# Kernel tuning notes

Hardware: AMD Instinct MI355X
Metric: run time of the kernel (lower is better)

## Reference

```python
import jax, jax.numpy as jnp
import numpy as np

N_NODES = 50000
N_EDGES = 600000
D = 128
THETA = (0.5, -1.0, 0.5)  # len(theta) must be 3 to match learnable_diag[3, in_feats]


def setup_inputs() -> dict:
    key = jax.random.key(0)
    k1, k2, k3, k4, k5 = jax.random.split(key, 5)
    feat = jax.random.normal(k1, (N_NODES, D), dtype=jnp.float32)
    edge_index = jax.random.randint(k2, (2, N_EDGES), 0, N_NODES)  # [src; dst]
    # learnable_diag = torch.rand(3, in_feats)
    diag = jax.random.uniform(k3, (3, D), dtype=jnp.float32)
    # nn.Linear(out_feats, out_feats) with xavier_uniform weight, zero bias
    limit = float(np.sqrt(6.0 / (D + D)))
    W = jax.random.uniform(k4, (D, D), dtype=jnp.float32, minval=-limit, maxval=limit)
    b = jnp.zeros((D,), dtype=jnp.float32)
    return {"feat": feat, "edge_index": edge_index, "diag": diag, "W": W, "b": b}


def reference(feat, edge_index, diag, W, b):
    src, dst = edge_index[0], edge_index[1]
    n = feat.shape[0]
    # in_degrees: count of incoming edges per node
    deg = jax.ops.segment_sum(jnp.ones_like(dst, dtype=feat.dtype), dst, num_segments=n)
    d_invsqrt = jnp.clip(deg, 1.0, None) ** -0.5  # [N]
    d_invsqrt = d_invsqrt[:, None]  # [N,1]

    h = (THETA[0] * feat) * diag[0]
    h = h @ W.T + b  # nn.Linear

    for k in range(1, len(THETA)):
        # unnLaplacian: feat - (A @ (feat * Dinv)) * Dinv * diag[k]
        msg = feat * d_invsqrt  # [N,D]
        agg = jax.ops.segment_sum(msg[src], dst, num_segments=n)  # SpMM: copy_u + sum
        feat = feat - agg * d_invsqrt * diag[k]
        h = h + THETA[k] * feat
    return h
```

## Files before the change

### kernel.cpp

```cpp
#include <hip/hip_runtime.h>

#define NN 50000
#define NE 600000
#define D  128
#define NBLK 196

typedef __attribute__((ext_vector_type(8))) short bf16x8;
typedef __attribute__((ext_vector_type(4))) float floatx4;

__device__ __forceinline__ unsigned short bf16_rne(float f) {
    union { float f; unsigned u; } v; v.f = f;
    unsigned r = v.u + 0x7FFFu + ((v.u >> 16) & 1u);
    return (unsigned short)(r >> 16);
}
__device__ __forceinline__ unsigned pack2(float a, float b) {
    return (unsigned)bf16_rne(a) | ((unsigned)bf16_rne(b) << 16);
}

__global__ __launch_bounds__(256) void hist_kernel(const int* __restrict__ dst,
                                                   int* __restrict__ deg_i) {
    int e = blockIdx.x * 256 + threadIdx.x;
    if (e < NE) atomicAdd(&deg_i[dst[e]], 1);
}

__global__ __launch_bounds__(256) void scan1_kernel(const int* __restrict__ deg_i,
                                                    int* __restrict__ row_ptr,
                                                    int* __restrict__ partials,
                                                    float* __restrict__ dinvf,
                                                    float* __restrict__ rdegf) {
    __shared__ int sh[256];
    int i = blockIdx.x * 256 + threadIdx.x;
    int dg = (i < NN) ? deg_i[i] : 0;
    if (i < NN) {
        float d = (float)dg;
        float dc = d > 1.0f ? d : 1.0f;
        dinvf[i] = rsqrtf(dc);
        rdegf[i] = sqrtf(dc);
    }
    sh[threadIdx.x] = dg;
    __syncthreads();
    #pragma unroll
    for (int off = 1; off < 256; off <<= 1) {
        int t = (threadIdx.x >= off) ? sh[threadIdx.x - off] : 0;
        __syncthreads();
        sh[threadIdx.x] += t;
        __syncthreads();
    }
    if (i < NN) row_ptr[i + 1] = sh[threadIdx.x];
    if (threadIdx.x == 255) partials[blockIdx.x] = sh[255];
}

__global__ __launch_bounds__(256) void scan2_kernel(int* __restrict__ partials) {
    __shared__ int sh[256];
    sh[threadIdx.x] = (threadIdx.x < NBLK) ? partials[threadIdx.x] : 0;
    __syncthreads();
    #pragma unroll
    for (int off = 1; off < 256; off <<= 1) {
        int t = (threadIdx.x >= off) ? sh[threadIdx.x - off] : 0;
        __syncthreads();
        sh[threadIdx.x] += t;
        __syncthreads();
    }
    if (threadIdx.x < NBLK) partials[threadIdx.x] = sh[threadIdx.x];
}

__global__ __launch_bounds__(256) void scan3_kernel(int* __restrict__ row_ptr,
                                                    const int* __restrict__ partials,
                                                    int* __restrict__ fillc) {
    int i = blockIdx.x * 256 + threadIdx.x;
    if (i < NN) {
        int add = (blockIdx.x > 0) ? partials[blockIdx.x - 1] : 0;
        row_ptr[i + 1] += add;
        fillc[i] = 0;
    }
    if (i == 0) row_ptr[0] = 0;
}

__global__ __launch_bounds__(256) void fill_kernel(const int* __restrict__ src,
                                                   const int* __restrict__ dst,
                                                   const int* __restrict__ row_ptr,
                                                   int* __restrict__ fillc,
                                                   int* __restrict__ csr) {
    int e = blockIdx.x * 256 + threadIdx.x;
    if (e < NE) {
        int t = dst[e];
        int pos = row_ptr[t] + atomicAdd(&fillc[t], 1);
        csr[pos] = src[e];
    }
}

__global__ __launch_bounds__(256) void wprep_kernel(const float* __restrict__ W,
                                                    const float* __restrict__ diag,
                                                    unsigned short* __restrict__ Wb) {
    int idx = blockIdx.x * 256 + threadIdx.x;
    int j = idx & 127;
    Wb[idx] = bf16_rne(0.5f * diag[j] * W[idx]);
}

__global__ __launch_bounds__(256) void gemm_mfma_kernel(const float* __restrict__ feat,
                                                        const unsigned short* __restrict__ Wb,
                                                        const float* __restrict__ b,
                                                        const float* __restrict__ dinvf,
                                                        unsigned short* __restrict__ featb_s,
                                                        float* __restrict__ out) {
    const int wv   = threadIdx.x >> 6;
    const int lane = threadIdx.x & 63;
    const int r16  = lane & 15;
    const int quad = lane >> 4;
    const int m0   = blockIdx.x * 64 + wv * 16;

    const int mrow = m0 + r16;
    const int mc   = (mrow < NN) ? mrow : (NN - 1);
    const float* arow = feat + (size_t)mc * D + quad * 8;
    const float di = dinvf[mc];

    bf16x8 afrag[4];
    #pragma unroll
    for (int kc = 0; kc < 4; ++kc) {
        const float4 f0 = *(const float4*)(arow + kc * 32);
        const float4 f1 = *(const float4*)(arow + kc * 32 + 4);
        bf16x8 a;
        a[0] = (short)bf16_rne(f0.x); a[1] = (short)bf16_rne(f0.y);
        a[2] = (short)bf16_rne(f0.z); a[3] = (short)bf16_rne(f0.w);
        a[4] = (short)bf16_rne(f1.x); a[5] = (short)bf16_rne(f1.y);
        a[6] = (short)bf16_rne(f1.z); a[7] = (short)bf16_rne(f1.w);
        afrag[kc] = a;
        if (mrow < NN) {
            uint4 st;
            st.x = pack2(f0.x * di, f0.y * di);
            st.y = pack2(f0.z * di, f0.w * di);
            st.z = pack2(f1.x * di, f1.y * di);
            st.w = pack2(f1.z * di, f1.w * di);
            *(uint4*)(featb_s + (size_t)mc * D + quad * 8 + kc * 32) = st;
        }
    }

    floatx4 acc[8];
    #pragma unroll
    for (int nt = 0; nt < 8; ++nt) acc[nt] = (floatx4)(0.0f);

    #pragma unroll
    for (int nt = 0; nt < 8; ++nt) {
        const unsigned short* brow = Wb + (size_t)(nt * 16 + r16) * D + quad * 8;
        #pragma unroll
        for (int kc = 0; kc < 4; ++kc) {
            const bf16x8 bfrag = *(const bf16x8*)(brow + kc * 32);
            acc[nt] = __builtin_amdgcn_mfma_f32_16x16x32_bf16(afrag[kc], bfrag, acc[nt], 0, 0, 0);
        }
    }

    #pragma unroll
    for (int nt = 0; nt < 8; ++nt) {
        const int d = nt * 16 + r16;
        const float bd = b[d];
        #pragma unroll
        for (int r = 0; r < 4; ++r) {
            const int i = m0 + quad * 4 + r;
            if (i < NN) out[(size_t)i * D + d] = acc[nt][r] + bd;
        }
    }
}

__device__ __forceinline__ float2 gather_acc(const unsigned short* __restrict__ rows,
                                             const int* __restrict__ csr,
                                             int e0, int e1, int lane) {
    float2 acc = make_float2(0.0f, 0.0f);
    for (int bse = e0; bse < e1; bse += 64) {
        int idx = bse + lane;
        int s = (idx < e1) ? csr[idx] : NN;
        int cnt8 = (min(64, e1 - bse) + 7) & ~7;
        for (int k = 0; k < cnt8; k += 8) {
            #pragma unroll
            for (int u = 0; u < 8; ++u) {
                int ss = __shfl(s, k + u);
                unsigned pv = *(const unsigned*)(rows + (size_t)ss * D + 2 * lane);
                acc.x += __uint_as_float(pv << 16);
                acc.y += __uint_as_float(pv & 0xFFFF0000u);
            }
        }
    }
    return acc;
}

__global__ __launch_bounds__(256) void gather1_kernel(const unsigned short* __restrict__ featb_s,
                                                      const int* __restrict__ csr,
                                                      const int* __restrict__ row_ptr,
                                                      const float* __restrict__ dinvf,
                                                      const float* __restrict__ diag,
                                                      const float* __restrict__ feat0,
                                                      unsigned int* __restrict__ feat1s) {
    const int node = blockIdx.x * 4 + (threadIdx.x >> 6);
    const int lane = threadIdx.x & 63;
    float2 acc = gather_acc(featb_s, csr, row_ptr[node], row_ptr[node + 1], lane);

    const size_t o2 = (size_t)node * (D / 2) + lane;
    const float di = dinvf[node];
    const float2 bs = *(const float2*)&feat0[2 * o2];
    const float2 dg = *(const float2*)&diag[D + 2 * lane];
    float rx = bs.x - acc.x * di * dg.x;
    float ry = bs.y - acc.y * di * dg.y;
    feat1s[o2] = pack2(rx * di, ry * di);
}

__global__ __launch_bounds__(256) void gather2_kernel(const unsigned short* __restrict__ feat1s,
                                                      const int* __restrict__ csr,
                                                      const int* __restrict__ row_ptr,
                                                      const float* __restrict__ dinvf,
                                                      const float* __restrict__ rdegf,
                                                      const float* __restrict__ diag,
                                                      float* __restrict__ outp) {
    const int node = blockIdx.x * 4 + (threadIdx.x >> 6);
    const int lane = threadIdx.x & 63;
    float2 acc = gather_acc(feat1s, csr, row_ptr[node], row_ptr[node + 1], lane);

    const size_t o2 = (size_t)node * (D / 2) + lane;
    const float di = dinvf[node];
    const float rd = rdegf[node];
    const unsigned bp = ((const unsigned*)feat1s)[o2];
    const float2 dg = *(const float2*)&diag[2 * D + 2 * lane];
    float bx = __uint_as_float(bp << 16) * rd;
    float by = __uint_as_float(bp & 0xFFFF0000u) * rd;
    float2 cur = *(const float2*)&outp[2 * o2];
    cur.x -= 0.5f * (bx + acc.x * di * dg.x);
    cur.y -= 0.5f * (by + acc.y * di * dg.y);
    *(float2*)&outp[2 * o2] = cur;
}

extern "C" void kernel_launch(void* const* d_in, const int* in_sizes, int n_in,
                              void* d_out, int out_size, void* d_ws, size_t ws_size,
                              hipStream_t stream) {
    const float* feat = (const float*)d_in[0];
    const int*   eidx = (const int*)d_in[1];
    const float* diag = (const float*)d_in[2];
    const float* W    = (const float*)d_in[3];
    const float* b    = (const float*)d_in[4];
    float* out = (float*)d_out;

    const int* src = eidx;
    const int* dst = eidx + NE;

    unsigned short* featb_s = (unsigned short*)d_ws;
    unsigned short* feat1s  = featb_s + (size_t)(NN + 1) * D;
    int*   csr      = (int*)(feat1s + (size_t)(NN + 1) * D);
    float* dinvf    = (float*)(csr + NE);
    float* rdegf    = dinvf + NN;
    int*   deg_i    = (int*)(rdegf + NN);
    int*   row_ptr  = deg_i + NN;
    int*   fillc    = row_ptr + NN + 2;
    int*   partials = fillc + NN;
    unsigned short* Wb = (unsigned short*)(partials + 256);

    hipMemsetAsync(deg_i, 0, (size_t)NN * sizeof(int), stream);
    hipMemsetAsync(featb_s + (size_t)NN * D, 0, D * sizeof(unsigned short), stream);
    hipMemsetAsync(feat1s  + (size_t)NN * D, 0, D * sizeof(unsigned short), stream);

    hist_kernel<<<(NE + 255) / 256, 256, 0, stream>>>(dst, deg_i);
    scan1_kernel<<<NBLK, 256, 0, stream>>>(deg_i, row_ptr, partials, dinvf, rdegf);
    scan2_kernel<<<1, 256, 0, stream>>>(partials);
    scan3_kernel<<<NBLK, 256, 0, stream>>>(row_ptr, partials, fillc);
    fill_kernel<<<(NE + 255) / 256, 256, 0, stream>>>(src, dst, row_ptr, fillc, csr);

    wprep_kernel<<<64, 256, 0, stream>>>(W, diag, Wb);

    gemm_mfma_kernel<<<(NN + 63) / 64, 256, 0, stream>>>(feat, Wb, b, dinvf, featb_s, out);

    gather1_kernel<<<NN / 4, 256, 0, stream>>>(featb_s, csr, row_ptr, dinvf, diag,
                                               feat, (unsigned int*)feat1s);
    gather2_kernel<<<NN / 4, 256, 0, stream>>>(feat1s, csr, row_ptr, dinvf, rdegf, diag, out);
}
```

Baseline: 235.3 us.

## Fuse memsets and scans into fewer kernels and split gathers by feature half

Replaces the three memsets and the weight-prep kernel with one prep kernel. It also merges the three-pass scan into a single-pass decoupled look-back scan that uses per-block descriptors. The two gather kernels now launch twice as many blocks: each wave handles half of the feature dimension, and its two 32-lane halves walk alternate edges before combining with a cross-lane shuffle. This cuts launch overhead and raises memory-level parallelism in the gathers, at the cost of reading the CSR twice and relying on inter-block spin-waiting in the scan.

```diff
diff --git a/kernel.cpp b/kernel.cpp
--- a/kernel.cpp
+++ b/kernel.cpp
@@ -17,19 +17,40 @@
     return (unsigned)bf16_rne(a) | ((unsigned)bf16_rne(b) << 16);
 }
 
+__global__ __launch_bounds__(256) void prep_kernel(const float* __restrict__ W,
+                                                   const float* __restrict__ diag,
+                                                   unsigned short* __restrict__ Wb,
+                                                   int* __restrict__ deg_i,
+                                                   int* __restrict__ fillc,
+                                                   unsigned long long* __restrict__ desc,
+                                                   unsigned int* __restrict__ zrow0,
+                                                   unsigned int* __restrict__ zrow1) {
+    int g = blockIdx.x * 256 + threadIdx.x;
+    if (g < NN) { deg_i[g] = 0; fillc[g] = 0; }
+    if (g < 16384) {
+        int j = g & 127;
+        Wb[g] = bf16_rne(0.5f * diag[j] * W[g]);
+    }
+    if (g < 256) desc[g] = 0ULL;
+    if (g < 64) { zrow0[g] = 0u; zrow1[g] = 0u; }
+}
+
 __global__ __launch_bounds__(256) void hist_kernel(const int* __restrict__ dst,
                                                    int* __restrict__ deg_i) {
     int e = blockIdx.x * 256 + threadIdx.x;
     if (e < NE) atomicAdd(&deg_i[dst[e]], 1);
 }
 
-__global__ __launch_bounds__(256) void scan1_kernel(const int* __restrict__ deg_i,
-                                                    int* __restrict__ row_ptr,
-                                                    int* __restrict__ partials,
-                                                    float* __restrict__ dinvf,
-                                                    float* __restrict__ rdegf) {
+__global__ __launch_bounds__(256) void scan_kernel(const int* __restrict__ deg_i,
+                                                   int* __restrict__ row_ptr,
+                                                   unsigned long long* __restrict__ desc,
+                                                   float* __restrict__ dinvf,
+                                                   float* __restrict__ rdegf) {
     __shared__ int sh[256];
-    int i = blockIdx.x * 256 + threadIdx.x;
+    __shared__ int exc_sh;
+    const int b = blockIdx.x;
+    const int t = threadIdx.x;
+    const int i = b * 256 + t;
     int dg = (i < NN) ? deg_i[i] : 0;
     if (i < NN) {
         float d = (float)dg;
@@ -37,42 +58,41 @@
         dinvf[i] = rsqrtf(dc);
         rdegf[i] = sqrtf(dc);
     }
-    sh[threadIdx.x] = dg;
+    sh[t] = dg;
     __syncthreads();
     #pragma unroll
     for (int off = 1; off < 256; off <<= 1) {
-        int t = (threadIdx.x >= off) ? sh[threadIdx.x - off] : 0;
+        int v = (t >= off) ? sh[t - off] : 0;
         __syncthreads();
-        sh[threadIdx.x] += t;
+        sh[t] += v;
         __syncthreads();
     }
-    if (i < NN) row_ptr[i + 1] = sh[threadIdx.x];
-    if (threadIdx.x == 255) partials[blockIdx.x] = sh[255];
-}
-
-__global__ __launch_bounds__(256) void scan2_kernel(int* __restrict__ partials) {
-    __shared__ int sh[256];
-    sh[threadIdx.x] = (threadIdx.x < NBLK) ? partials[threadIdx.x] : 0;
+    if (t == 0) {
+        const int agg = sh[255];
+        if (b == 0) {
+            exc_sh = 0;
+            atomicExch(&desc[0], (2ULL << 32) | (unsigned)agg);
+        } else {
+            atomicExch(&desc[b], (1ULL << 32) | (unsigned)agg);
+            long long running = 0;
+            int p = b - 1;
+            for (;;) {
+                unsigned long long v;
+                do {
+                    v = atomicAdd(&desc[p], 0ULL);
+                    if ((v >> 32) == 0) __builtin_amdgcn_s_sleep(1);
+                } while ((v >> 32) == 0);
+                running += (long long)(unsigned)v;
+                if ((v >> 32) == 2ULL) break;
+                --p;
+            }
+            exc_sh = (int)running;
+            atomicExch(&desc[b], (2ULL << 32) | (unsigned)(running + agg));
+        }
+    }
     __syncthreads();
-    #pragma unroll
-    for (int off = 1; off < 256; off <<= 1) {
-        int t = (threadIdx.x >= off) ? sh[threadIdx.x - off] : 0;
-        __syncthreads();
-        sh[threadIdx.x] += t;
-        __syncthreads();
-    }
-    if (threadIdx.x < NBLK) partials[threadIdx.x] = sh[threadIdx.x];
-}
-
-__global__ __launch_bounds__(256) void scan3_kernel(int* __restrict__ row_ptr,
-                                                    const int* __restrict__ partials,
-                                                    int* __restrict__ fillc) {
-    int i = blockIdx.x * 256 + threadIdx.x;
-    if (i < NN) {
-        int add = (blockIdx.x > 0) ? partials[blockIdx.x - 1] : 0;
-        row_ptr[i + 1] += add;
-        fillc[i] = 0;
-    }
+    const int exc = exc_sh;
+    if (i < NN) row_ptr[i + 1] = sh[t] + exc;
     if (i == 0) row_ptr[0] = 0;
 }
 
@@ -87,14 +107,6 @@
         int pos = row_ptr[t] + atomicAdd(&fillc[t], 1);
         csr[pos] = src[e];
     }
-}
-
-__global__ __launch_bounds__(256) void wprep_kernel(const float* __restrict__ W,
-                                                    const float* __restrict__ diag,
-                                                    unsigned short* __restrict__ Wb) {
-    int idx = blockIdx.x * 256 + threadIdx.x;
-    int j = idx & 127;
-    Wb[idx] = bf16_rne(0.5f * diag[j] * W[idx]);
 }
 
 __global__ __launch_bounds__(256) void gemm_mfma_kernel(const float* __restrict__ feat,
@@ -161,9 +173,11 @@
     }
 }
 
-__device__ __forceinline__ float2 gather_acc(const unsigned short* __restrict__ rows,
-                                             const int* __restrict__ csr,
-                                             int e0, int e1, int lane) {
+__device__ __forceinline__ float2 gather_half(const unsigned short* __restrict__ rows,
+                                              const int* __restrict__ csr,
+                                              int e0, int e1, int lane, int half) {
+    const unsigned short* rbase = rows + half * 64 + 2 * (lane & 31);
+    const int sub = lane >> 5;
     float2 acc = make_float2(0.0f, 0.0f);
     for (int bse = e0; bse < e1; bse += 64) {
         int idx = bse + lane;
@@ -171,14 +185,16 @@
         int cnt8 = (min(64, e1 - bse) + 7) & ~7;
         for (int k = 0; k < cnt8; k += 8) {
             #pragma unroll
-            for (int u = 0; u < 8; ++u) {
-                int ss = __shfl(s, k + u);
-                unsigned pv = *(const unsigned*)(rows + (size_t)ss * D + 2 * lane);
+            for (int u = 0; u < 8; u += 2) {
+                int ss = __shfl(s, k + u + sub);
+                unsigned pv = *(const unsigned*)(rbase + (size_t)ss * D);
                 acc.x += __uint_as_float(pv << 16);
                 acc.y += __uint_as_float(pv & 0xFFFF0000u);
             }
         }
     }
+    acc.x += __shfl_xor(acc.x, 32);
+    acc.y += __shfl_xor(acc.y, 32);
     return acc;
 }
 
@@ -189,17 +205,20 @@
                                                       const float* __restrict__ diag,
                                                       const float* __restrict__ feat0,
                                                       unsigned int* __restrict__ feat1s) {
-    const int node = blockIdx.x * 4 + (threadIdx.x >> 6);
+    const int half = (blockIdx.x >= NN / 4) ? 1 : 0;
+    const int node = (blockIdx.x - half * (NN / 4)) * 4 + (threadIdx.x >> 6);
     const int lane = threadIdx.x & 63;
-    float2 acc = gather_acc(featb_s, csr, row_ptr[node], row_ptr[node + 1], lane);
-
-    const size_t o2 = (size_t)node * (D / 2) + lane;
-    const float di = dinvf[node];
-    const float2 bs = *(const float2*)&feat0[2 * o2];
-    const float2 dg = *(const float2*)&diag[D + 2 * lane];
-    float rx = bs.x - acc.x * di * dg.x;
-    float ry = bs.y - acc.y * di * dg.y;
-    feat1s[o2] = pack2(rx * di, ry * di);
+    float2 acc = gather_half(featb_s, csr, row_ptr[node], row_ptr[node + 1], lane, half);
+
+    if (lane < 32) {
+        const int dd = half * 64 + 2 * lane;
+        const float di = dinvf[node];
+        const float2 bs = *(const float2*)&feat0[(size_t)node * D + dd];
+        const float2 dg = *(const float2*)&diag[D + dd];
+        float rx = bs.x - acc.x * di * dg.x;
+        float ry = bs.y - acc.y * di * dg.y;
+        feat1s[(size_t)node * (D / 2) + half * 32 + lane] = pack2(rx * di, ry * di);
+    }
 }
 
 __global__ __launch_bounds__(256) void gather2_kernel(const unsigned short* __restrict__ feat1s,
@@ -209,21 +228,24 @@
                                                       const float* __restrict__ rdegf,
                                                       const float* __restrict__ diag,
                                                       float* __restrict__ outp) {
-    const int node = blockIdx.x * 4 + (threadIdx.x >> 6);
+    const int half = (blockIdx.x >= NN / 4) ? 1 : 0;
+    const int node = (blockIdx.x - half * (NN / 4)) * 4 + (threadIdx.x >> 6);
     const int lane = threadIdx.x & 63;
-    float2 acc = gather_acc(feat1s, csr, row_ptr[node], row_ptr[node + 1], lane);
-
-    const size_t o2 = (size_t)node * (D / 2) + lane;
-    const float di = dinvf[node];
-    const float rd = rdegf[node];
-    const unsigned bp = ((const unsigned*)feat1s)[o2];
-    const float2 dg = *(const float2*)&diag[2 * D + 2 * lane];
-    float bx = __uint_as_float(bp << 16) * rd;
-    float by = __uint_as_float(bp & 0xFFFF0000u) * rd;
-    float2 cur = *(const float2*)&outp[2 * o2];
-    cur.x -= 0.5f * (bx + acc.x * di * dg.x);
-    cur.y -= 0.5f * (by + acc.y * di * dg.y);
-    *(float2*)&outp[2 * o2] = cur;
+    float2 acc = gather_half(feat1s, csr, row_ptr[node], row_ptr[node + 1], lane, half);
+
+    if (lane < 32) {
+        const int dd = half * 64 + 2 * lane;
+        const float di = dinvf[node];
+        const float rd = rdegf[node];
+        const unsigned bp = ((const unsigned*)feat1s)[(size_t)node * (D / 2) + half * 32 + lane];
+        const float2 dg = *(const float2*)&diag[2 * D + dd];
+        float bx = __uint_as_float(bp << 16) * rd;
+        float by = __uint_as_float(bp & 0xFFFF0000u) * rd;
+        float2 cur = *(const float2*)&outp[(size_t)node * D + dd];
+        cur.x -= 0.5f * (bx + acc.x * di * dg.x);
+        cur.y -= 0.5f * (by + acc.y * di * dg.y);
+        *(float2*)&outp[(size_t)node * D + dd] = cur;
+    }
 }
 
 extern "C" void kernel_launch(void* const* d_in, const int* in_sizes, int n_in,
@@ -247,24 +269,20 @@
     int*   deg_i    = (int*)(rdegf + NN);
     int*   row_ptr  = deg_i + NN;
     int*   fillc    = row_ptr + NN + 2;
-    int*   partials = fillc + NN;
-    unsigned short* Wb = (unsigned short*)(partials + 256);
-
-    hipMemsetAsync(deg_i, 0, (size_t)NN * sizeof(int), stream);
-    hipMemsetAsync(featb_s + (size_t)NN * D, 0, D * sizeof(unsigned short), stream);
-    hipMemsetAsync(feat1s  + (size_t)NN * D, 0, D * sizeof(unsigned short), stream);
-
+    unsigned long long* desc = (unsigned long long*)(fillc + NN);
+    unsigned short* Wb = (unsigned short*)(desc + 256);
+
+    prep_kernel<<<NBLK, 256, 0, stream>>>(W, diag, Wb, deg_i, fillc, desc,
+                                          (unsigned int*)(featb_s + (size_t)NN * D),
+                                          (unsigned int*)(feat1s + (size_t)NN * D));
     hist_kernel<<<(NE + 255) / 256, 256, 0, stream>>>(dst, deg_i);
-    scan1_kernel<<<NBLK, 256, 0, stream>>>(deg_i, row_ptr, partials, dinvf, rdegf);
-    scan2_kernel<<<1, 256, 0, stream>>>(partials);
-    scan3_kernel<<<NBLK, 256, 0, stream>>>(row_ptr, partials, fillc);
+    scan_kernel<<<NBLK, 256, 0, stream>>>(deg_i, row_ptr, desc, dinvf, rdegf);
     fill_kernel<<<(NE + 255) / 256, 256, 0, stream>>>(src, dst, row_ptr, fillc, csr);
 
-    wprep_kernel<<<64, 256, 0, stream>>>(W, diag, Wb);
-
     gemm_mfma_kernel<<<(NN + 63) / 64, 256, 0, stream>>>(feat, Wb, b, dinvf, featb_s, out);
 
-    gather1_kernel<<<NN / 4, 256, 0, stream>>>(featb_s, csr, row_ptr, dinvf, diag,
-                                               feat, (unsigned int*)feat1s);
-    gather2_kernel<<<NN / 4, 256, 0, stream>>>(feat1s, csr, row_ptr, dinvf, rdegf, diag, out);
-}
+    gather1_kernel<<<2 * (NN / 4), 256, 0, stream>>>(featb_s, csr, row_ptr, dinvf, diag,
+                                                     feat, (unsigned int*)feat1s);
+    gather2_kernel<<<2 * (NN / 4), 256, 0, stream>>>(feat1s, csr, row_ptr, dinvf, rdegf,
+                                                     diag, out);
+}
```

Result: slower. 247.8 us (+5.3%).
